# Performance work log

Measured on AMD Instinct MI355X. Metric: run time of the kernel, lower is better.

Reference implementation:

```python
import jax, jax.numpy as jnp
import numpy as np

MARGIN = 1.0  # from init_kwargs
B, H, W, P = 64, 512, 640, 100000


def setup_inputs() -> dict:
    key = jax.random.key(0)
    k0, k1, k2, k3, k4, k5 = jax.random.split(key, 6)
    return {
        "inp": jax.random.normal(k0, (B, 1, H, W), dtype=jnp.float32),
        "x_A": jax.random.randint(k1, (B, P), 0, W, dtype=jnp.int32),
        "y_A": jax.random.randint(k2, (B, P), 0, H, dtype=jnp.int32),
        "x_B": jax.random.randint(k3, (B, P), 0, W, dtype=jnp.int32),
        "y_B": jax.random.randint(k4, (B, P), 0, H, dtype=jnp.int32),
        "ordinal": jax.random.randint(k5, (B, P), 0, 3, dtype=jnp.int32),
    }


def reference(inp, x_A, y_A, x_B, y_B, ordinal):
    # inp: [B,1,H,W]; point coords: [B,P]; ordinal in {0,1,2} -> gt in {-1,0,1}
    depth = inp[:, 0]                                   # [B,H,W]
    bidx = jnp.arange(depth.shape[0])[:, None]          # [B,1]
    z_A = depth[bidx, y_A, x_A]                         # [B,P] gather
    z_B = depth[bidx, y_B, x_B]                         # [B,P] gather
    gt = (ordinal - 1).astype(depth.dtype)              # {-1,0,1}
    mask = jnp.abs(gt)
    zd = z_A - z_B
    m = jnp.asarray(MARGIN, depth.dtype)
    # ordered pairs: log(1+exp(-min(gt*zd, m))); equal pairs: max(zd^2, m^2)
    loss = mask * jnp.log(1.0 + jnp.exp(-jnp.minimum(gt * zd, m))) \
         + (1.0 - mask) * jnp.maximum(zd * zd, m * m)
    n_point_total = depth.shape[0] * x_A.shape[1]
    return jnp.sum(loss) / n_point_total
```

## Files before the change

### kernel.cpp

```cpp
#include <hip/hip_runtime.h>


constexpr int B = 64;
constexpr int H = 512;
constexpr int W = 640;
constexpr int P = 100000;
constexpr int HWSZ = H * W;
constexpr int N4B = P / 4;
constexpr int NCHUNK = 8;
constexpr int C4 = N4B / NCHUNK;
constexpr int THREADS = 512;
constexpr int NWAVE = 8;
constexpr int SLOTS = 7;
constexpr int NG = SLOTS * 8;
constexpr int NE = C4 * 8;
constexpr int TE = 4096;
constexpr int T = HWSZ / TE;
constexpr int NBLK = B * NCHUNK;
constexpr float INV_N = 1.0f / (float)(B * P);
constexpr float MARGIN = 1.0f;

typedef int vint4 __attribute__((ext_vector_type(4)));
typedef float vfloat4 __attribute__((ext_vector_type(4)));

__device__ __forceinline__ float loss_from(float za, float zb, int od) {
    float zd = za - zb;
    float gt = (float)(od - 1);
    float mask = fabsf(gt);
    float t = fminf(gt * zd, MARGIN);
    float l_rank = __logf(1.0f + __expf(-t));
    float l_eq = fmaxf(zd * zd, MARGIN * MARGIN);
    return mask * l_rank + (1.0f - mask) * l_eq;
}

__global__ __launch_bounds__(THREADS) void rdc_sweep(
        const float* __restrict__ depth,
        const vint4* __restrict__ xA, const vint4* __restrict__ yA,
        const vint4* __restrict__ xB, const vint4* __restrict__ yB,
        const vint4* __restrict__ ord,
        float* __restrict__ partials) {
    __shared__ unsigned cells[NE];
    __shared__ float tiles[2][TE];
    __shared__ unsigned hist[NWAVE][T];
    __shared__ unsigned cur[NWAVE][T];
    __shared__ unsigned startB[T + 1];
    __shared__ float wsum[NWAVE];

    const int j = blockIdx.x;
    const int x = j & 7;
    const int g = j >> 3;
    const int chunk = g & 7;
    const int b = ((g >> 3) << 3) + x;

    const int tid = threadIdx.x;
    const int lane = tid & 63;
    const int wid = tid >> 6;

    const float* dimg = depth + (size_t)b * HWSZ;

    const vfloat4* s40 = (const vfloat4*)dimg;
    vfloat4 ld0a = s40[tid];
    vfloat4 ld0b = s40[THREADS + tid];

    ((unsigned*)hist)[tid] = 0u;
    if (tid < NWAVE * T - THREADS) ((unsigned*)hist)[THREADS + tid] = 0u;

    const int base4 = b * N4B + chunk * C4;
    const bool v6 = (tid < C4 - (SLOTS - 1) * THREADS);
    unsigned key[NG];
    int pack[SLOTS];
    #pragma unroll
    for (int i = 0; i < SLOTS; ++i) {
        int c = i * THREADS + tid;
        if (c > C4 - 1) c = C4 - 1;
        int idx = base4 + c;
        vint4 xa = __builtin_nontemporal_load(&xA[idx]);
        vint4 ya = __builtin_nontemporal_load(&yA[idx]);
        vint4 xb = __builtin_nontemporal_load(&xB[idx]);
        vint4 yb = __builtin_nontemporal_load(&yB[idx]);
        vint4 od = __builtin_nontemporal_load(&ord[idx]);
        key[i*8+0] = ya.x * W + xa.x;  key[i*8+1] = yb.x * W + xb.x;
        key[i*8+2] = ya.y * W + xa.y;  key[i*8+3] = yb.y * W + xb.y;
        key[i*8+4] = ya.z * W + xa.z;  key[i*8+5] = yb.z * W + xb.z;
        key[i*8+6] = ya.w * W + xa.w;  key[i*8+7] = yb.w * W + xb.w;
        pack[i] = (od.x & 3) | ((od.y & 3) << 2) | ((od.z & 3) << 4)
                | ((od.w & 3) << 6);
    }
    __syncthreads();

    #pragma unroll
    for (int k = 0; k < NG; ++k) {
        if (k < 48 || v6) {
            unsigned bin = key[k] >> 12;
            atomicAdd(&hist[wid][bin], 1u);
        }
    }
    __syncthreads();

    if (wid == 0) {
        unsigned h0[NWAVE], h1[NWAVE];
        unsigned sum0 = 0, sum1 = 0;
        const int b0 = 2 * lane, b1 = 2 * lane + 1;
        if (lane < T / 2) {
            #pragma unroll
            for (int w = 0; w < NWAVE; ++w) h0[w] = hist[w][b0];
            #pragma unroll
            for (int w = 0; w < NWAVE; ++w) h1[w] = hist[w][b1];
            #pragma unroll
            for (int w = 0; w < NWAVE; ++w) { unsigned t_ = h0[w]; h0[w] = sum0; sum0 += t_; }
            #pragma unroll
            for (int w = 0; w < NWAVE; ++w) { unsigned t_ = h1[w]; h1[w] = sum1; sum1 += t_; }
        }
        unsigned pair = sum0 + sum1;
        unsigned inc = pair;
        #pragma unroll
        for (int d = 1; d < 64; d <<= 1) {
            unsigned n = __shfl_up(inc, d, 64);
            if (lane >= d) inc += n;
        }
        unsigned ex = inc - pair;
        if (lane < T / 2) {
            unsigned s0 = ex, s1 = ex + sum0;
            startB[b0] = s0;
            startB[b1] = s1;
            if (lane == T / 2 - 1) startB[T] = s1 + sum1;
            #pragma unroll
            for (int w = 0; w < NWAVE; ++w) {
                cur[w][b0] = s0 + h0[w];
                cur[w][b1] = s1 + h1[w];
            }
        }
    }
    __syncthreads();

    #pragma unroll
    for (int k = 0; k < NG; ++k) {
        if (k < 48 || v6) {
            unsigned kk = key[k];
            unsigned bin = kk >> 12;
            unsigned rel = kk & (unsigned)(TE - 1);
            unsigned pos = atomicAdd(&cur[wid][bin], 1u);
            cells[pos] = rel;
            key[k] = pos;
        } else {
            key[k] = 0u;
        }
    }

    vfloat4 r0, r1;
    {
        vfloat4* d4 = (vfloat4*)&tiles[0][0];
        d4[tid] = ld0a;
        d4[THREADS + tid] = ld0b;
        const vfloat4* s4 = (const vfloat4*)(dimg + TE);
        r0 = s4[tid];
        r1 = s4[THREADS + tid];
    }
    __syncthreads();

    #pragma unroll 1
    for (int t = 0; t < T; ++t) {
        if (t + 1 < T) {
            vfloat4* d4 = (vfloat4*)&tiles[(t + 1) & 1][0];
            d4[tid] = r0;
            d4[THREADS + tid] = r1;
        }
        if (t + 2 < T) {
            const vfloat4* s4 = (const vfloat4*)(dimg + (size_t)(t + 2) * TE);
            r0 = s4[tid];
            r1 = s4[THREADS + tid];
        }
        const float* tb = &tiles[t & 1][0];
        unsigned s = startB[t];
        unsigned e = startB[t + 1];
        for (unsigned u = s + tid; u < e; u += THREADS) {
            unsigned rel = cells[u];
            cells[u] = __float_as_uint(tb[rel]);
        }
        __syncthreads();
    }

    float acc = 0.0f;
    #pragma unroll
    for (int i = 0; i < SLOTS; ++i) {
        float li = 0.0f;
        #pragma unroll
        for (int q = 0; q < 4; ++q) {
            float za = __uint_as_float(cells[key[i*8 + 2*q]]);
            float zb = __uint_as_float(cells[key[i*8 + 2*q + 1]]);
            li += loss_from(za, zb, (pack[i] >> (2 * q)) & 3);
        }
        if (i == SLOTS - 1) li *= (v6 ? 1.0f : 0.0f);
        acc += li;
    }

    #pragma unroll
    for (int off2 = 32; off2 > 0; off2 >>= 1)
        acc += __shfl_down(acc, off2, 64);
    if (lane == 0) wsum[wid] = acc;
    __syncthreads();
    if (wid == 0) {
        float v = (lane < NWAVE) ? wsum[lane] : 0.0f;
        #pragma unroll
        for (int off2 = 4; off2 > 0; off2 >>= 1)
            v += __shfl_down(v, off2, 64);
        if (lane == 0) partials[j] = v;
    }
}

__global__ __launch_bounds__(256) void rdc_finalize(
        const float* __restrict__ partials, float* __restrict__ out, int n) {
    float acc = 0.0f;
    for (int k = threadIdx.x; k < n; k += 256)
        acc += partials[k];
    #pragma unroll
    for (int off = 32; off > 0; off >>= 1)
        acc += __shfl_down(acc, off, 64);
    __shared__ float wsum[4];
    int lane = threadIdx.x & 63;
    int wid  = threadIdx.x >> 6;
    if (lane == 0) wsum[wid] = acc;
    __syncthreads();
    if (wid == 0 && lane == 0)
        out[0] = (wsum[0] + wsum[1] + wsum[2] + wsum[3]) * INV_N;
}

extern "C" void kernel_launch(void* const* d_in, const int* in_sizes, int n_in,
                              void* d_out, int out_size, void* d_ws, size_t ws_size,
                              hipStream_t stream) {
    const float* depth = (const float*)d_in[0];
    const vint4* xA = (const vint4*)d_in[1];
    const vint4* yA = (const vint4*)d_in[2];
    const vint4* xB = (const vint4*)d_in[3];
    const vint4* yB = (const vint4*)d_in[4];
    const vint4* ord = (const vint4*)d_in[5];
    float* out = (float*)d_out;

    float* partials = (float*)d_ws;
    rdc_sweep<<<NBLK, THREADS, 0, stream>>>(depth, xA, yA, xB, yB, ord, partials);
    rdc_finalize<<<1, 256, 0, stream>>>(partials, out, NBLK);
}
```

Baseline: 290.5 us.

## Halve chunks per image and split cell buffer into two passes over image halves

New measurement: 271.5 us. 6.5% less time.

```diff
diff --git a/kernel.cpp b/kernel.cpp
--- a/kernel.cpp
+++ b/kernel.cpp
@@ -7,16 +7,19 @@
 constexpr int P = 100000;
 constexpr int HWSZ = H * W;
 constexpr int N4B = P / 4;
-constexpr int NCHUNK = 8;
+constexpr int NCHUNK = 4;
 constexpr int C4 = N4B / NCHUNK;
 constexpr int THREADS = 512;
 constexpr int NWAVE = 8;
-constexpr int SLOTS = 7;
+constexpr int SLOTS = 13;
 constexpr int NG = SLOTS * 8;
 constexpr int NE = C4 * 8;
 constexpr int TE = 4096;
 constexpr int T = HWSZ / TE;
+constexpr int THALF = T / 2;
+constexpr int CCAP = 27008;
 constexpr int NBLK = B * NCHUNK;
+constexpr int VTAIL = C4 - (SLOTS - 1) * THREADS;
 constexpr float INV_N = 1.0f / (float)(B * P);
 constexpr float MARGIN = 1.0f;
 
@@ -39,18 +42,19 @@
         const vint4* __restrict__ xB, const vint4* __restrict__ yB,
         const vint4* __restrict__ ord,
         float* __restrict__ partials) {
-    __shared__ unsigned cells[NE];
+    __shared__ unsigned cells[CCAP];
     __shared__ float tiles[2][TE];
     __shared__ unsigned hist[NWAVE][T];
     __shared__ unsigned cur[NWAVE][T];
     __shared__ unsigned startB[T + 1];
+    __shared__ unsigned endA_s;
     __shared__ float wsum[NWAVE];
 
     const int j = blockIdx.x;
     const int x = j & 7;
     const int g = j >> 3;
-    const int chunk = g & 7;
-    const int b = ((g >> 3) << 3) + x;
+    const int chunk = g & 3;
+    const int b = ((g >> 2) << 3) + x;
 
     const int tid = threadIdx.x;
     const int lane = tid & 63;
@@ -58,17 +62,13 @@
 
     const float* dimg = depth + (size_t)b * HWSZ;
 
-    const vfloat4* s40 = (const vfloat4*)dimg;
-    vfloat4 ld0a = s40[tid];
-    vfloat4 ld0b = s40[THREADS + tid];
-
     ((unsigned*)hist)[tid] = 0u;
     if (tid < NWAVE * T - THREADS) ((unsigned*)hist)[THREADS + tid] = 0u;
 
     const int base4 = b * N4B + chunk * C4;
-    const bool v6 = (tid < C4 - (SLOTS - 1) * THREADS);
+    const bool v12 = (tid < VTAIL);
     unsigned key[NG];
-    int pack[SLOTS];
+    unsigned pack[SLOTS];
     #pragma unroll
     for (int i = 0; i < SLOTS; ++i) {
         int c = i * THREADS + tid;
@@ -86,13 +86,24 @@
         pack[i] = (od.x & 3) | ((od.y & 3) << 2) | ((od.z & 3) << 4)
                 | ((od.w & 3) << 6);
     }
-    __syncthreads();
-
+
+    vfloat4 t0a, t0b, r0, r1;
+    {
+        const vfloat4* s40 = (const vfloat4*)dimg;
+        t0a = s40[tid];  t0b = s40[THREADS + tid];
+        const vfloat4* s41 = (const vfloat4*)(dimg + TE);
+        r0 = s41[tid];   r1 = s41[THREADS + tid];
+    }
+    __syncthreads();
+
+    unsigned mm[4] = {0u, 0u, 0u, 0u};
     #pragma unroll
     for (int k = 0; k < NG; ++k) {
-        if (k < 48 || v6) {
+        bool valid = (k < (SLOTS - 1) * 8) || v12;
+        if (valid) {
             unsigned bin = key[k] >> 12;
             atomicAdd(&hist[wid][bin], 1u);
+            if (bin < (unsigned)THALF) mm[k >> 5] |= (1u << (k & 31));
         }
     }
     __syncthreads();
@@ -119,8 +130,11 @@
             if (lane >= d) inc += n;
         }
         unsigned ex = inc - pair;
+        unsigned e40 = __shfl(ex, THALF / 2, 64);
+        if (lane == 0) endA_s = e40;
         if (lane < T / 2) {
-            unsigned s0 = ex, s1 = ex + sum0;
+            unsigned rb = (b0 >= THALF) ? e40 : 0u;
+            unsigned s0 = ex - rb, s1 = ex + sum0 - rb;
             startB[b0] = s0;
             startB[b1] = s1;
             if (lane == T / 2 - 1) startB[T] = s1 + sum1;
@@ -135,31 +149,43 @@
 
     #pragma unroll
     for (int k = 0; k < NG; ++k) {
-        if (k < 48 || v6) {
+        if ((mm[k >> 5] >> (k & 31)) & 1u) {
             unsigned kk = key[k];
             unsigned bin = kk >> 12;
-            unsigned rel = kk & (unsigned)(TE - 1);
             unsigned pos = atomicAdd(&cur[wid][bin], 1u);
-            cells[pos] = rel;
+            cells[pos] = kk & (unsigned)(TE - 1);
             key[k] = pos;
-        } else {
-            key[k] = 0u;
-        }
-    }
-
-    vfloat4 r0, r1;
+        }
+    }
     {
         vfloat4* d4 = (vfloat4*)&tiles[0][0];
-        d4[tid] = ld0a;
-        d4[THREADS + tid] = ld0b;
-        const vfloat4* s4 = (const vfloat4*)(dimg + TE);
-        r0 = s4[tid];
-        r1 = s4[THREADS + tid];
+        d4[tid] = t0a;
+        d4[THREADS + tid] = t0b;
     }
     __syncthreads();
 
     #pragma unroll 1
     for (int t = 0; t < T; ++t) {
+        if (t == THALF) {
+            #pragma unroll
+            for (int k = 0; k < NG; ++k) {
+                if ((mm[k >> 5] >> (k & 31)) & 1u)
+                    key[k] = cells[key[k]];
+            }
+            __syncthreads();
+            #pragma unroll
+            for (int k = 0; k < NG; ++k) {
+                bool valid = (k < (SLOTS - 1) * 8) || v12;
+                if (valid && !((mm[k >> 5] >> (k & 31)) & 1u)) {
+                    unsigned kk = key[k];
+                    unsigned bin = kk >> 12;
+                    unsigned pos = atomicAdd(&cur[wid][bin], 1u);
+                    cells[pos] = kk & (unsigned)(TE - 1);
+                    key[k] = pos;
+                }
+            }
+            __syncthreads();
+        }
         if (t + 1 < T) {
             vfloat4* d4 = (vfloat4*)&tiles[(t + 1) & 1][0];
             d4[tid] = r0;
@@ -172,7 +198,7 @@
         }
         const float* tb = &tiles[t & 1][0];
         unsigned s = startB[t];
-        unsigned e = startB[t + 1];
+        unsigned e = (t == THALF - 1) ? endA_s : startB[t + 1];
         for (unsigned u = s + tid; u < e; u += THREADS) {
             unsigned rel = cells[u];
             cells[u] = __float_as_uint(tb[rel]);
@@ -180,17 +206,23 @@
         __syncthreads();
     }
 
+    #pragma unroll
+    for (int k = 0; k < NG; ++k) {
+        bool valid = (k < (SLOTS - 1) * 8) || v12;
+        if (valid && !((mm[k >> 5] >> (k & 31)) & 1u))
+            key[k] = cells[key[k]];
+    }
     float acc = 0.0f;
     #pragma unroll
     for (int i = 0; i < SLOTS; ++i) {
         float li = 0.0f;
         #pragma unroll
         for (int q = 0; q < 4; ++q) {
-            float za = __uint_as_float(cells[key[i*8 + 2*q]]);
-            float zb = __uint_as_float(cells[key[i*8 + 2*q + 1]]);
-            li += loss_from(za, zb, (pack[i] >> (2 * q)) & 3);
-        }
-        if (i == SLOTS - 1) li *= (v6 ? 1.0f : 0.0f);
+            float za = __uint_as_float(key[i*8 + 2*q]);
+            float zb = __uint_as_float(key[i*8 + 2*q + 1]);
+            li += loss_from(za, zb, (int)((pack[i] >> (2 * q)) & 3u));
+        }
+        if (i == SLOTS - 1) li *= (v12 ? 1.0f : 0.0f);
         acc += li;
     }
 
```
